# Kernel optimization log

Measured on AMD Instinct MI355X. Metric: run time of the kernel, lower is better.

## Reference

```python
import jax, jax.numpy as jnp
import numpy as np

N_NODES = 100000
N_EDGES = 1_600_000
D_IN = 128
D_OUT = 128


def setup_inputs() -> dict:
    key = jax.random.key(0)
    k1, k2, k3 = jax.random.split(key, 3)
    input_matrix = jax.random.normal(k1, (N_NODES, D_IN), dtype=jnp.float32)
    adjacency_coo_matrix = jax.random.randint(k2, (2, N_EDGES), 0, N_NODES, dtype=jnp.int64)
    # xavier-uniform-style init for the weight matrix
    limit = float(np.sqrt(6.0 / (D_IN + D_OUT)))
    weights_matrix = jax.random.uniform(k3, (D_IN, D_OUT), dtype=jnp.float32, minval=-limit, maxval=limit)
    return {
        "input_matrix": input_matrix,
        "adjacency_coo_matrix": adjacency_coo_matrix,
        "weights_matrix": weights_matrix,
    }


def reference(input_matrix, adjacency_coo_matrix, weights_matrix):
    # Edge-wise gathers (the irregular-access pattern from the torch code)
    src_idx = adjacency_coo_matrix[0]
    dst_idx = adjacency_coo_matrix[1]
    neighbors = input_matrix[dst_idx]  # [E, D_IN] gather of neighbor features
    # Mean-aggregate neighbor features onto each src node
    agg = jax.ops.segment_sum(neighbors, src_idx, num_segments=N_NODES)  # [N, D_IN]
    deg = jax.ops.segment_sum(jnp.ones((neighbors.shape[0],), dtype=input_matrix.dtype),
                              src_idx, num_segments=N_NODES)  # [N]
    mean_agg = agg / jnp.maximum(deg, 1.0)[:, None]
    # Linear transform with the layer weight matrix
    out = mean_agg @ weights_matrix  # [N, D_OUT]
    return out
```

## Files before the change

### kernel.cpp

```cpp
#include <hip/hip_runtime.h>

#define NN 100000
#define NE 1600000
#define DD 128
#define CAP 64
#define SLICE_N 12500
#define FILL_BLOCKS 2048
#define BPS (FILL_BLOCKS / 8)
#define NGRP (NE / 4)
#define GEMM_BLOCKS ((NN + 63) / 64)
#define LDSP 136

typedef __bf16 bf16x8 __attribute__((ext_vector_type(8)));
typedef float  f32x4  __attribute__((ext_vector_type(4)));
typedef unsigned int u32x4 __attribute__((ext_vector_type(4)));

__device__ __forceinline__ unsigned int f2bf(float f) {
    unsigned int u = __float_as_uint(f);
    return (u + 0x7FFFu + ((u >> 16) & 1u)) >> 16;
}
__device__ __forceinline__ float bflo(unsigned int u) { return __uint_as_float(u << 16); }
__device__ __forceinline__ float bfhi(unsigned int u) { return __uint_as_float(u & 0xFFFF0000u); }

__global__ __launch_bounds__(256) void k_prep(const float* __restrict__ W,
                                              unsigned short* __restrict__ wtb,
                                              int* __restrict__ cnt)
{
    const int idx = blockIdx.x * 256 + (int)threadIdx.x;
    const int k = idx >> 7, n = idx & 127;
    wtb[n * DD + k] = (unsigned short)f2bf(W[idx]);
    int4* c4 = (int4*)cnt;
    for (int i = idx; i < NN / 4; i += DD * DD) c4[i] = make_int4(0, 0, 0, 0);
}

__global__ __launch_bounds__(256, 8) void k_fused(const int* __restrict__ adj,
                                                  int* __restrict__ cnt,
                                                  int* __restrict__ edge_dst,
                                                  const float* __restrict__ x,
                                                  const unsigned short* __restrict__ wtb,
                                                  unsigned short* __restrict__ y)
{
    __shared__ unsigned short ytile[64 * LDSP];

    const int b   = (int)blockIdx.x;
    const int tid = (int)threadIdx.x;
    const int wave = tid >> 6;
    const int lane = tid & 63;
    const int quad = lane >> 4;
    const int l16  = lane & 15;
    const int mbase = b * 64 + wave * 16;
    const int m = mbase + l16;

    f32x4 af[8];
    const bool amask = (b < GEMM_BLOCKS) && (m < NN);
    if (amask) {
        const float* arow = x + (size_t)m * DD + quad * 8;
        #pragma unroll
        for (int ks = 0; ks < 4; ++ks) {
            af[2 * ks + 0] = __builtin_nontemporal_load((const f32x4*)(arow + ks * 32));
            af[2 * ks + 1] = __builtin_nontemporal_load((const f32x4*)(arow + ks * 32 + 4));
        }
    }

    {
        const int slice = b & 7;
        const int w     = b >> 3;
        const int lo    = slice * SLICE_N;
        const u32x4* src4 = (const u32x4*)adj;
        const u32x4* dst4 = (const u32x4*)(adj + NE);
        const int stride  = BPS * 256;

        for (int g = w * 256 + tid; g < NGRP; g += stride) {
            const u32x4 s4 = __builtin_nontemporal_load(src4 + g);
            const u32x4 d4 = __builtin_nontemporal_load(dst4 + g);
            int sv[4], dv[4], slot[4];
            #pragma unroll
            for (int j = 0; j < 4; ++j) { sv[j] = (int)s4[j]; dv[j] = (int)d4[j]; }
            #pragma unroll
            for (int j = 0; j < 4; ++j) {
                slot[j] = ((unsigned)(sv[j] - lo) < (unsigned)SLICE_N)
                          ? atomicAdd(&cnt[sv[j]], 1) : CAP;
            }
            #pragma unroll
            for (int j = 0; j < 4; ++j) {
                if (slot[j] < CAP)
                    edge_dst[(size_t)sv[j] * CAP + slot[j]] = dv[j];
            }
        }
    }

    if (b >= GEMM_BLOCKS) return;

    bf16x8 a[4];
    if (amask) {
        #pragma unroll
        for (int ks = 0; ks < 4; ++ks) {
            const f32x4 f0 = af[2 * ks + 0];
            const f32x4 f1 = af[2 * ks + 1];
            u32x4 p;
            p[0] = f2bf(f0[0]) | (f2bf(f0[1]) << 16);
            p[1] = f2bf(f0[2]) | (f2bf(f0[3]) << 16);
            p[2] = f2bf(f1[0]) | (f2bf(f1[1]) << 16);
            p[3] = f2bf(f1[2]) | (f2bf(f1[3]) << 16);
            a[ks] = __builtin_bit_cast(bf16x8, p);
        }
    } else {
        const u32x4 z = 0;
        #pragma unroll
        for (int ks = 0; ks < 4; ++ks) a[ks] = __builtin_bit_cast(bf16x8, z);
    }

    unsigned short* lrow = ytile + wave * 16 * LDSP;

    #pragma unroll
    for (int nt = 0; nt < 8; ++nt) {
        f32x4 c = {0.f, 0.f, 0.f, 0.f};
        const unsigned short* bcol = wtb + (nt * 16 + l16) * DD + quad * 8;
        #pragma unroll
        for (int ks = 0; ks < 4; ++ks) {
            const bf16x8 bb = __builtin_bit_cast(bf16x8, *(const uint4*)(bcol + ks * 32));
            c = __builtin_amdgcn_mfma_f32_16x16x32_bf16(a[ks], bb, c, 0, 0, 0);
        }
        #pragma unroll
        for (int r = 0; r < 4; ++r)
            lrow[(quad * 4 + r) * LDSP + nt * 16 + l16] = (unsigned short)f2bf(c[r]);
    }

    __syncthreads();

    const int r16   = lane >> 2;
    const int ch    = lane & 3;
    const int growr = b * 64 + wave * 16 + r16;
    if (growr < NN) {
        const unsigned short* lsrc = ytile + (wave * 16 + r16) * LDSP + ch * 32;
        unsigned short* gdst = y + (size_t)growr * DD + ch * 32;
        *(uint4*)(gdst + 0)  = *(const uint4*)(lsrc + 0);
        *(uint4*)(gdst + 8)  = *(const uint4*)(lsrc + 8);
        *(uint4*)(gdst + 16) = *(const uint4*)(lsrc + 16);
        *(uint4*)(gdst + 24) = *(const uint4*)(lsrc + 24);
    }
}

__global__ __launch_bounds__(256) void k_agg2(const unsigned short* __restrict__ y,
                                              const int* __restrict__ cnt,
                                              const int* __restrict__ edge_dst,
                                              float* __restrict__ out)
{
    const int n    = blockIdx.x * 4 + ((int)threadIdx.x >> 6);
    const int lane = (int)threadIdx.x & 63;
    const int eg   = lane >> 4;
    const int h    = lane & 15;
    int deg = cnt[n];
    if (deg > CAP) deg = CAP;
    const int* el = edge_dst + (size_t)n * CAP;

    float acc[8] = {0.f,0.f,0.f,0.f,0.f,0.f,0.f,0.f};

    #define ACC(p) do {                                         \
        acc[0] += bflo((p).x); acc[1] += bfhi((p).x);           \
        acc[2] += bflo((p).y); acc[3] += bfhi((p).y);           \
        acc[4] += bflo((p).z); acc[5] += bfhi((p).z);           \
        acc[6] += bflo((p).w); acc[7] += bfhi((p).w);           \
    } while (0)

    int i = eg;
    for (; i + 12 < deg; i += 16) {
        const int d0 = el[i];
        const int d1 = el[i + 4];
        const int d2 = el[i + 8];
        const int d3 = el[i + 12];
        const uint4 p0 = *(const uint4*)(y + (size_t)d0 * DD + h * 8);
        const uint4 p1 = *(const uint4*)(y + (size_t)d1 * DD + h * 8);
        const uint4 p2 = *(const uint4*)(y + (size_t)d2 * DD + h * 8);
        const uint4 p3 = *(const uint4*)(y + (size_t)d3 * DD + h * 8);
        ACC(p0); ACC(p1); ACC(p2); ACC(p3);
    }
    for (; i + 4 < deg; i += 8) {
        const int d0 = el[i];
        const int d1 = el[i + 4];
        const uint4 p0 = *(const uint4*)(y + (size_t)d0 * DD + h * 8);
        const uint4 p1 = *(const uint4*)(y + (size_t)d1 * DD + h * 8);
        ACC(p0); ACC(p1);
    }
    for (; i < deg; i += 4) {
        const int d0 = el[i];
        const uint4 p0 = *(const uint4*)(y + (size_t)d0 * DD + h * 8);
        ACC(p0);
    }
    #undef ACC

    #pragma unroll
    for (int j = 0; j < 8; ++j) {
        acc[j] += __shfl_xor(acc[j], 16, 64);
        acc[j] += __shfl_xor(acc[j], 32, 64);
    }

    if (eg == 0) {
        const float inv = 1.0f / fmaxf((float)deg, 1.0f);
        float* o = out + (size_t)n * DD + h * 8;
        float4 w0 = {acc[0]*inv, acc[1]*inv, acc[2]*inv, acc[3]*inv};
        float4 w1 = {acc[4]*inv, acc[5]*inv, acc[6]*inv, acc[7]*inv};
        *(float4*)(o + 0) = w0;
        *(float4*)(o + 4) = w1;
    }
}

extern "C" void kernel_launch(void* const* d_in, const int* in_sizes, int n_in,
                              void* d_out, int out_size, void* d_ws, size_t ws_size,
                              hipStream_t stream) {
    const float* x   = (const float*)d_in[0];
    const int*   adj = (const int*)d_in[1];
    const float* W   = (const float*)d_in[2];
    float* out = (float*)d_out;

    unsigned short* y   = (unsigned short*)d_ws;
    unsigned short* wtb = y + (size_t)NN * DD;
    int* cnt      = (int*)(wtb + DD * DD);
    int* edge_dst = cnt + NN;

    k_prep <<<DD * DD / 256, 256, 0, stream>>>(W, wtb, cnt);
    k_fused<<<FILL_BLOCKS, 256, 0, stream>>>(adj, cnt, edge_dst, x, wtb, y);
    k_agg2 <<<NN / 4, 256, 0, stream>>>(y, cnt, edge_dst, out);
}
```

Baseline: 254.3 us.

## Fill edge buckets in one pass with one edge group per thread

Drops the eight-way source-slice partitioning of the edge-bucketing pass. Previously each of 2048 blocks read its share of the edge list but kept only edges whose source fell in its slice, so the full adjacency list was read eight times. Now each GEMM block handles exactly 256 contiguous groups of four edges with no filtering, and the grid shrinks to the GEMM block count. This cuts the redundant adjacency reads and the per-edge filtering. In exchange, the atomics and bucket writes are scattered over all nodes instead of one slice at a time, so counter and bucket accesses lose cache locality.

```diff
diff --git a/kernel.cpp b/kernel.cpp
--- a/kernel.cpp
+++ b/kernel.cpp
@@ -4,9 +4,6 @@
 #define NE 1600000
 #define DD 128
 #define CAP 64
-#define SLICE_N 12500
-#define FILL_BLOCKS 2048
-#define BPS (FILL_BLOCKS / 8)
 #define NGRP (NE / 4)
 #define GEMM_BLOCKS ((NN + 63) / 64)
 #define LDSP 136
@@ -42,8 +39,8 @@
 {
     __shared__ unsigned short ytile[64 * LDSP];
 
-    const int b   = (int)blockIdx.x;
-    const int tid = (int)threadIdx.x;
+    const int b    = (int)blockIdx.x;
+    const int tid  = (int)threadIdx.x;
     const int wave = tid >> 6;
     const int lane = tid & 63;
     const int quad = lane >> 4;
@@ -52,7 +49,7 @@
     const int m = mbase + l16;
 
     f32x4 af[8];
-    const bool amask = (b < GEMM_BLOCKS) && (m < NN);
+    const bool amask = (m < NN);
     if (amask) {
         const float* arow = x + (size_t)m * DD + quad * 8;
         #pragma unroll
@@ -63,33 +60,20 @@
     }
 
     {
-        const int slice = b & 7;
-        const int w     = b >> 3;
-        const int lo    = slice * SLICE_N;
-        const u32x4* src4 = (const u32x4*)adj;
-        const u32x4* dst4 = (const u32x4*)(adj + NE);
-        const int stride  = BPS * 256;
-
-        for (int g = w * 256 + tid; g < NGRP; g += stride) {
-            const u32x4 s4 = __builtin_nontemporal_load(src4 + g);
-            const u32x4 d4 = __builtin_nontemporal_load(dst4 + g);
-            int sv[4], dv[4], slot[4];
+        const int g = b * 256 + tid;
+        if (g < NGRP) {
+            const u32x4 s4 = __builtin_nontemporal_load((const u32x4*)adj + g);
+            const u32x4 d4 = __builtin_nontemporal_load((const u32x4*)(adj + NE) + g);
+            int slot[4];
             #pragma unroll
-            for (int j = 0; j < 4; ++j) { sv[j] = (int)s4[j]; dv[j] = (int)d4[j]; }
+            for (int j = 0; j < 4; ++j)
+                slot[j] = atomicAdd(&cnt[(int)s4[j]], 1);
             #pragma unroll
-            for (int j = 0; j < 4; ++j) {
-                slot[j] = ((unsigned)(sv[j] - lo) < (unsigned)SLICE_N)
-                          ? atomicAdd(&cnt[sv[j]], 1) : CAP;
-            }
-            #pragma unroll
-            for (int j = 0; j < 4; ++j) {
+            for (int j = 0; j < 4; ++j)
                 if (slot[j] < CAP)
-                    edge_dst[(size_t)sv[j] * CAP + slot[j]] = dv[j];
-            }
-        }
-    }
-
-    if (b >= GEMM_BLOCKS) return;
+                    edge_dst[(size_t)(int)s4[j] * CAP + slot[j]] = (int)d4[j];
+        }
+    }
 
     bf16x8 a[4];
     if (amask) {
@@ -219,6 +203,6 @@
     int* edge_dst = cnt + NN;
 
     k_prep <<<DD * DD / 256, 256, 0, stream>>>(W, wtb, cnt);
-    k_fused<<<FILL_BLOCKS, 256, 0, stream>>>(adj, cnt, edge_dst, x, wtb, y);
+    k_fused<<<GEMM_BLOCKS, 256, 0, stream>>>(adj, cnt, edge_dst, x, wtb, y);
     k_agg2 <<<NN / 4, 256, 0, stream>>>(y, cnt, edge_dst, out);
 }
```

Result: slower. 267.8 us (+5.3%).
